# Kernel tuning notes

Hardware: AMD Instinct MI355X
Metric: run time of the kernel (lower is better)

Reference implementation:

```python
import jax, jax.numpy as jnp
import numpy as np

CELL = 14
NC = 80
BPC = 3
IMG = 448.0
CS = IMG / CELL  # cell pixel size
CLASS_SCALE = 1.0
OBJECT_SCALE = 1.0
NOOBJECT_SCALE = 0.5
COORD_SCALE = 5.0
EPS = 1e-9

# base_boxes[y, x, b, :] = (x*CS, y*CS, 0, 0)
_gy, _gx = jnp.meshgrid(jnp.arange(CELL, dtype=jnp.float32), jnp.arange(CELL, dtype=jnp.float32), indexing='ij')
BASE = jnp.broadcast_to(jnp.stack([_gx * CS, _gy * CS, jnp.zeros_like(_gx), jnp.zeros_like(_gx)], axis=-1)[:, :, None, :], (CELL, CELL, BPC, 4))
MULT = jnp.array([CS, CS, IMG, IMG], dtype=jnp.float32)


def _ciou(boxes1, box2):
    # boxes1: [S,S,BPC,4] (cx,cy,w,h); box2: [4]
    b1_cx, b1_cy, b1_w, b1_h = boxes1[..., 0], boxes1[..., 1], boxes1[..., 2], boxes1[..., 3]
    b2_cx, b2_cy, b2_w, b2_h = box2[0], box2[1], box2[2], box2[3]
    b1_x1, b1_y1, b1_x2, b1_y2 = b1_cx - b1_w / 2, b1_cy - b1_h / 2, b1_cx + b1_w / 2, b1_cy + b1_h / 2
    b2_x1, b2_y1, b2_x2, b2_y2 = b2_cx - b2_w / 2, b2_cy - b2_h / 2, b2_cx + b2_w / 2, b2_cy + b2_h / 2
    inter = jnp.clip(jnp.minimum(b1_x2, b2_x2) - jnp.maximum(b1_x1, b2_x1), 0) * \
            jnp.clip(jnp.minimum(b1_y2, b2_y2) - jnp.maximum(b1_y1, b2_y1), 0)
    union = b1_w * b1_h + b2_w * b2_h - inter
    iou = inter / (union + EPS)
    center_distance = (b1_cx - b2_cx) ** 2 + (b1_cy - b2_cy) ** 2
    # faithful to original (uses center/size components for the enclosing box)
    enclose_left = jnp.minimum(boxes1[..., 0], box2[0])
    enclose_right = jnp.maximum(boxes1[..., 2], box2[2])
    enclose_top = jnp.minimum(boxes1[..., 1], box2[1])
    enclose_bottom = jnp.maximum(boxes1[..., 3], box2[3])
    enclose_diag = (enclose_right - enclose_left) ** 2 + (enclose_bottom - enclose_top) ** 2
    v = (4.0 / jnp.pi ** 2) * (jnp.arctan(b2_w / (b2_h + EPS)) - jnp.arctan(b1_w / (b1_h + EPS))) ** 2
    alpha = jax.lax.stop_gradient(v / (1 - iou + v + EPS))
    return iou - center_distance / (enclose_diag + EPS) - alpha * v  # [S,S,BPC]


def _l2(t):
    return 0.5 * jnp.sum(t * t)


def _per_object_loss(predict, label):
    # predict: [S,S,NC+5*BPC], label: [5]
    gy = jnp.arange(CELL, dtype=jnp.float32)[:, None]
    gx = jnp.arange(CELL, dtype=jnp.float32)[None, :]
    x, y, w, h = label[0], label[1], label[2], label[3]
    min_x = jnp.floor((x - w / 2) / CS)
    max_x = jnp.minimum(jnp.ceil((x + w / 2) / CS), CELL)
    min_y = jnp.floor((y - h / 2) / CS)
    max_y = jnp.minimum(jnp.ceil((y + h / 2) / CS), CELL)
    object_mask = ((gx >= min_x) & (gx < max_x) & (gy >= min_y) & (gy < max_y)).astype(jnp.float32)
    cx, cy = jnp.floor(x / CS), jnp.floor(y / CS)
    center_mask = ((gx == cx) & (gy == cy)).astype(jnp.float32)

    pboxes = predict[:, :, NC + BPC:].reshape(CELL, CELL, BPC, 4) * MULT + BASE
    iou = _ciou(pboxes, label[:4])                     # [S,S,BPC]
    C = iou * center_mask[..., None]
    I = (iou >= jnp.max(iou, axis=-1, keepdims=True)).astype(jnp.float32) * center_mask[..., None]
    no_I = 1.0 - I
    p_C = predict[:, :, NC:NC + BPC]

    sqrt_w, sqrt_h = jnp.sqrt(jnp.abs(w)), jnp.sqrt(jnp.abs(h))
    p_x, p_y = pboxes[..., 0], pboxes[..., 1]
    p_sqrt_w = jnp.sqrt(jnp.clip(pboxes[..., 2], 0.0, IMG))
    p_sqrt_h = jnp.sqrt(jnp.clip(pboxes[..., 3], 0.0, IMG))

    P = jax.nn.one_hot(label[4].astype(jnp.int32), NC, dtype=jnp.float32)
    p_P = predict[:, :, :NC]

    class_loss = _l2(object_mask[..., None] * (p_P - P)) * CLASS_SCALE
    object_loss = _l2(I * (p_C - C)) * OBJECT_SCALE
    noobject_loss = _l2(no_I * p_C) * NOOBJECT_SCALE
    coord_loss = (_l2(I * (p_x - x) / CS) + _l2(I * (p_y - y) / CS)
                  + _l2(I * (p_sqrt_w - sqrt_w)) / IMG + _l2(I * (p_sqrt_h - sqrt_h)) / IMG) * COORD_SCALE
    return class_loss + object_loss + noobject_loss + coord_loss


def setup_inputs() -> dict:
    key = jax.random.key(0)
    k1, k2, k3, k4, k5 = jax.random.split(key, 5)
    B, M = 1024, 30
    predicts = jax.random.normal(k1, (B, CELL, CELL, NC + 5 * BPC), dtype=jnp.float32) * 0.1
    xy = jax.random.uniform(k2, (B, M, 2), minval=60.0, maxval=IMG - 60.0)
    wh = jax.random.uniform(k3, (B, M, 2), minval=10.0, maxval=100.0)
    cls = jax.random.randint(k4, (B, M, 1), 0, NC).astype(jnp.float32)
    labels = jnp.concatenate([xy, wh, cls], axis=-1)
    objects_num = jax.random.randint(k5, (B,), 1, M + 1).astype(jnp.int32)
    return {"predicts": predicts, "labels": labels, "objects_num": objects_num}


def reference(predicts, labels, objects_num):
    B, M = labels.shape[0], labels.shape[1]
    per_batch = jax.vmap(lambda p, ls: jax.vmap(lambda l: _per_object_loss(p, l))(ls))
    losses = per_batch(predicts, labels)  # [B, M]
    mask = (jnp.arange(M)[None, :] < objects_num[:, None]).astype(jnp.float32)
    return jnp.sum(losses * mask) / B
```

## Files before the change

kernel.cpp:

```cpp
#include <hip/hip_runtime.h>
#include <math.h>

#define CELLN 14
#define NCELLS 196
#define NCLS 80
#define NCH 95
#define NDW (NCELLS * NCH)
#define NF4 (NDW / 4)

__global__ __launch_bounds__(256, 4) void yolo_loss_kernel(
    const float* __restrict__ predicts,
    const float* __restrict__ labels,
    const int* __restrict__ objects_num,
    float* __restrict__ out,
    int M, float invB)
{
    __shared__ float s_half[NCELLS + 1];
    __shared__ float s_red[4];

    const int img  = blockIdx.x;
    const int tid  = threadIdx.x;
    const int lane = tid & 63;
    const int wid  = tid >> 6;
    const float inv32 = 1.0f / 32.0f;

    const float*  gpred = predicts + (size_t)img * NDW;
    const float4* gp4   = (const float4*)gpred;
    const int n = objects_num[img];

    for (int i = tid; i < NCELLS + 1; i += 256) s_half[i] = 0.0f;
    __syncthreads();

    float acc = 0.0f;
    for (int g = (tid >> 3); g < n; g += 32) {
        const int r = tid & 7;
        const float* lab = labels + ((size_t)img * M + g) * 5;
        const float x = lab[0], y = lab[1], w = lab[2], h = lab[3];

        int min_x = max(0, (int)floorf((x - w * 0.5f) * inv32));
        int max_x = min(CELLN, (int)ceilf((x + w * 0.5f) * inv32));
        int min_y = max(0, (int)floorf((y - h * 0.5f) * inv32));
        int max_y = min(CELLN, (int)ceilf((y + h * 0.5f) * inv32));
        int nx = max_x - min_x;
        int ncell = nx * (max_y - min_y);

        if (r == 0) acc += 0.5f * (float)ncell;
        for (int p = r; p < ncell; p += 8) {
            int cell = (min_y + p / nx) * CELLN + (min_x + p % nx);
            atomicAdd(&s_half[cell], 0.5f);
        }
    }
    __syncthreads();

    const float qn = 0.25f * (float)n;
    float acc2 = 0.0f;
    #pragma unroll
    for (int i = 0; i < 19; ++i) {
        int f = tid + (i << 8);
        if (f < NF4) {
            float4 v4 = gp4[f];
            unsigned idx  = (unsigned)f << 2;
            unsigned cell = idx / 95u;
            unsigned ch   = idx - cell * 95u;
            float vv[4] = {v4.x, v4.y, v4.z, v4.w};
            #pragma unroll
            for (int k = 0; k < 4; ++k) {
                float cnt = s_half[cell];
                float c = (ch < 80u) ? cnt : ((ch < 83u) ? qn : 0.0f);
                float v = vv[k];
                if (k & 1) acc2 = fmaf(c * v, v, acc2);
                else       acc  = fmaf(c * v, v, acc);
                ++ch;
                if (ch == 95u) { ch = 0u; ++cell; }
            }
        }
    }
    acc += acc2;

    for (int g = (tid >> 3); g < n; g += 32) {
        const int r = tid & 7;
        const float* lab = labels + ((size_t)img * M + g) * 5;
        const float x = lab[0], y = lab[1], w = lab[2], h = lab[3];
        const int cls = (int)lab[4];

        int min_x = max(0, (int)floorf((x - w * 0.5f) * inv32));
        int max_x = min(CELLN, (int)ceilf((x + w * 0.5f) * inv32));
        int min_y = max(0, (int)floorf((y - h * 0.5f) * inv32));
        int max_y = min(CELLN, (int)ceilf((y + h * 0.5f) * inv32));
        int nx = max_x - min_x;
        int ncell = nx * (max_y - min_y);

        float csum = 0.0f;
        for (int p = r; p < ncell; p += 8) {
            int cell = (min_y + p / nx) * CELLN + (min_x + p % nx);
            csum += gpred[cell * NCH + cls];
        }
        acc -= csum;
    }

    for (int o = tid; o < n; o += 256) {
        const float* lab = labels + ((size_t)img * M + o) * 5;
        const float x = lab[0], y = lab[1], w = lab[2], h = lab[3];

        int cx = (int)floorf(x * inv32);
        int cy = (int)floorf(y * inv32);
        const float* cp = gpred + (cy * CELLN + cx) * NCH;
        float bx = (float)cx * 32.0f;
        float by = (float)cy * 32.0f;

        float pC[3], ciou[3], pxv[3], pyv[3], pwv[3], phv[3];
        #pragma unroll
        for (int b = 0; b < 3; ++b) {
            pC[b] = cp[NCLS + b];
            float px = cp[83 + 4*b] * 32.0f + bx;
            float py = cp[84 + 4*b] * 32.0f + by;
            float pw = cp[85 + 4*b] * 448.0f;
            float ph = cp[86 + 4*b] * 448.0f;
            pxv[b] = px; pyv[b] = py; pwv[b] = pw; phv[b] = ph;
            float iw = fminf(px + pw*0.5f, x + w*0.5f) - fmaxf(px - pw*0.5f, x - w*0.5f);
            float ih = fminf(py + ph*0.5f, y + h*0.5f) - fmaxf(py - ph*0.5f, y - h*0.5f);
            iw = fmaxf(iw, 0.0f); ih = fmaxf(ih, 0.0f);
            float inter = iw * ih;
            float uni = pw*ph + w*h - inter;
            float iou = inter / (uni + 1e-9f);
            float cd = (px - x)*(px - x) + (py - y)*(py - y);
            float el = fminf(px, x), er = fmaxf(pw, w);
            float et = fminf(py, y), eb = fmaxf(ph, h);
            float ed = (er - el)*(er - el) + (eb - et)*(eb - et);
            float da = atanf(w / (h + 1e-9f)) - atanf(pw / (ph + 1e-9f));
            float v = 0.40528473456935108577f * da * da;
            float alpha = v / (1.0f - iou + v + 1e-9f);
            ciou[b] = iou - cd / (ed + 1e-9f) - alpha * v;
        }
        float mx = fmaxf(ciou[0], fmaxf(ciou[1], ciou[2]));
        float sqw = sqrtf(fabsf(w)), sqh = sqrtf(fabsf(h));
        float sel_obj = 0.0f, sel_pc2 = 0.0f, coord = 0.0f;
        #pragma unroll
        for (int b = 0; b < 3; ++b) {
            if (ciou[b] >= mx) {
                float d = pC[b] - ciou[b];
                sel_obj += d * d;
                sel_pc2 += pC[b] * pC[b];
                float dx = (pxv[b] - x) * inv32;
                float dy = (pyv[b] - y) * inv32;
                float psw = sqrtf(fminf(fmaxf(pwv[b], 0.0f), 448.0f));
                float psh = sqrtf(fminf(fmaxf(phv[b], 0.0f), 448.0f));
                float dw = psw - sqw, dh = psh - sqh;
                coord += dx*dx + dy*dy + (dw*dw + dh*dh) * (1.0f/448.0f);
            }
        }
        acc += 0.5f * sel_obj - 0.25f * sel_pc2 + 2.5f * coord;
    }

    #pragma unroll
    for (int off = 32; off; off >>= 1) acc += __shfl_down(acc, off);
    if (lane == 0) s_red[wid] = acc;
    __syncthreads();
    if (tid == 0) {
        atomicAdd(out, (s_red[0] + s_red[1] + s_red[2] + s_red[3]) * invB);
    }
}

extern "C" void kernel_launch(void* const* d_in, const int* in_sizes, int n_in,
                              void* d_out, int out_size, void* d_ws, size_t ws_size,
                              hipStream_t stream) {
    const float* predicts = (const float*)d_in[0];
    const float* labels   = (const float*)d_in[1];
    const int*   objn     = (const int*)d_in[2];
    float* out = (float*)d_out;

    const int B = in_sizes[2];
    const int M = in_sizes[1] / (B * 5);

    yolo_loss_kernel<<<dim3(B), dim3(256), 0, stream>>>(
        predicts, labels, objn, out, M, 1.0f / (float)B);
}
```

Before: 119.1 us.

## Split each image across two blocks, prefetch predictions, reduce via workspace

Each image is now handled by two blocks, each covering half of the prediction tensor. Each block issues all of its float4 loads into registers up front, before building the shared cell-count table, so the memory traffic overlaps with the atomic setup. Label-driven class and box terms run only in the first half-block, which leaves the two blocks unevenly loaded, and both halves rebuild the shared count table. Per-block partials are written to a workspace and summed by a second single-block kernel instead of a global atomic, which adds one kernel launch.

```diff
diff --git a/kernel.cpp b/kernel.cpp
--- a/kernel.cpp
+++ b/kernel.cpp
@@ -7,18 +7,21 @@
 #define NCH 95
 #define NDW (NCELLS * NCH)
 #define NF4 (NDW / 4)
-
-__global__ __launch_bounds__(256, 4) void yolo_loss_kernel(
+#define HALF0 2328
+
+__global__ __launch_bounds__(256, 4) void yolo_main(
     const float* __restrict__ predicts,
     const float* __restrict__ labels,
     const int* __restrict__ objects_num,
-    float* __restrict__ out,
-    int M, float invB)
+    float* __restrict__ ws,
+    int M)
 {
-    __shared__ float s_half[NCELLS + 1];
+    __shared__ float s_half[NCELLS + 2];
     __shared__ float s_red[4];
 
-    const int img  = blockIdx.x;
+    const int blk  = blockIdx.x;
+    const int img  = blk >> 1;
+    const int sub  = blk & 1;
     const int tid  = threadIdx.x;
     const int lane = tid & 63;
     const int wid  = tid >> 6;
@@ -28,12 +31,23 @@
     const float4* gp4   = (const float4*)gpred;
     const int n = objects_num[img];
 
-    for (int i = tid; i < NCELLS + 1; i += 256) s_half[i] = 0.0f;
+    const int base = sub ? HALF0 : 0;
+    const int C    = sub ? (NF4 - HALF0) : HALF0;
+    const int f0   = base + tid;
+    float4 r[10];
+    #pragma unroll
+    for (int i = 0; i < 9; ++i)
+        r[i] = gp4[f0 + i * 256];
+    const bool ok9 = (tid + 9 * 256) < C;
+    r[9] = gp4[ok9 ? (f0 + 9 * 256) : base];
+    if (!ok9) r[9] = make_float4(0.f, 0.f, 0.f, 0.f);
+
+    for (int i = tid; i < NCELLS + 2; i += 256) s_half[i] = 0.0f;
     __syncthreads();
 
     float acc = 0.0f;
     for (int g = (tid >> 3); g < n; g += 32) {
-        const int r = tid & 7;
+        const int r8 = tid & 7;
         const float* lab = labels + ((size_t)img * M + g) * 5;
         const float x = lab[0], y = lab[1], w = lab[2], h = lab[3];
 
@@ -44,8 +58,8 @@
         int nx = max_x - min_x;
         int ncell = nx * (max_y - min_y);
 
-        if (r == 0) acc += 0.5f * (float)ncell;
-        for (int p = r; p < ncell; p += 8) {
+        if (r8 == 0 && sub == 0) acc += 0.5f * (float)ncell;
+        for (int p = r8; p < ncell; p += 8) {
             int cell = (min_y + p / nx) * CELLN + (min_x + p % nx);
             atomicAdd(&s_half[cell], 0.5f);
         }
@@ -55,110 +69,122 @@
     const float qn = 0.25f * (float)n;
     float acc2 = 0.0f;
     #pragma unroll
-    for (int i = 0; i < 19; ++i) {
-        int f = tid + (i << 8);
-        if (f < NF4) {
-            float4 v4 = gp4[f];
-            unsigned idx  = (unsigned)f << 2;
-            unsigned cell = idx / 95u;
-            unsigned ch   = idx - cell * 95u;
-            float vv[4] = {v4.x, v4.y, v4.z, v4.w};
-            #pragma unroll
-            for (int k = 0; k < 4; ++k) {
-                float cnt = s_half[cell];
-                float c = (ch < 80u) ? cnt : ((ch < 83u) ? qn : 0.0f);
-                float v = vv[k];
-                if (k & 1) acc2 = fmaf(c * v, v, acc2);
-                else       acc  = fmaf(c * v, v, acc);
-                ++ch;
-                if (ch == 95u) { ch = 0u; ++cell; }
-            }
+    for (int i = 0; i < 10; ++i) {
+        unsigned fg = (unsigned)(f0 - base + i * 256);
+        fg += (unsigned)base;
+        if (i == 9) fg = min(fg, (unsigned)(NF4 - 1));
+        unsigned idx  = fg << 2;
+        unsigned cell = idx / 95u;
+        unsigned ch   = idx - cell * 95u;
+        float vv[4] = {r[i].x, r[i].y, r[i].z, r[i].w};
+        #pragma unroll
+        for (int k = 0; k < 4; ++k) {
+            float cnt = s_half[cell];
+            float c = (ch < 80u) ? cnt : ((ch < 83u) ? qn : 0.0f);
+            float v = vv[k];
+            if (k & 1) acc2 = fmaf(c * v, v, acc2);
+            else       acc  = fmaf(c * v, v, acc);
+            ++ch;
+            if (ch == 95u) { ch = 0u; ++cell; }
         }
     }
     acc += acc2;
 
-    for (int g = (tid >> 3); g < n; g += 32) {
-        const int r = tid & 7;
-        const float* lab = labels + ((size_t)img * M + g) * 5;
-        const float x = lab[0], y = lab[1], w = lab[2], h = lab[3];
-        const int cls = (int)lab[4];
-
-        int min_x = max(0, (int)floorf((x - w * 0.5f) * inv32));
-        int max_x = min(CELLN, (int)ceilf((x + w * 0.5f) * inv32));
-        int min_y = max(0, (int)floorf((y - h * 0.5f) * inv32));
-        int max_y = min(CELLN, (int)ceilf((y + h * 0.5f) * inv32));
-        int nx = max_x - min_x;
-        int ncell = nx * (max_y - min_y);
-
-        float csum = 0.0f;
-        for (int p = r; p < ncell; p += 8) {
-            int cell = (min_y + p / nx) * CELLN + (min_x + p % nx);
-            csum += gpred[cell * NCH + cls];
-        }
-        acc -= csum;
-    }
-
-    for (int o = tid; o < n; o += 256) {
-        const float* lab = labels + ((size_t)img * M + o) * 5;
-        const float x = lab[0], y = lab[1], w = lab[2], h = lab[3];
-
-        int cx = (int)floorf(x * inv32);
-        int cy = (int)floorf(y * inv32);
-        const float* cp = gpred + (cy * CELLN + cx) * NCH;
-        float bx = (float)cx * 32.0f;
-        float by = (float)cy * 32.0f;
-
-        float pC[3], ciou[3], pxv[3], pyv[3], pwv[3], phv[3];
-        #pragma unroll
-        for (int b = 0; b < 3; ++b) {
-            pC[b] = cp[NCLS + b];
-            float px = cp[83 + 4*b] * 32.0f + bx;
-            float py = cp[84 + 4*b] * 32.0f + by;
-            float pw = cp[85 + 4*b] * 448.0f;
-            float ph = cp[86 + 4*b] * 448.0f;
-            pxv[b] = px; pyv[b] = py; pwv[b] = pw; phv[b] = ph;
-            float iw = fminf(px + pw*0.5f, x + w*0.5f) - fmaxf(px - pw*0.5f, x - w*0.5f);
-            float ih = fminf(py + ph*0.5f, y + h*0.5f) - fmaxf(py - ph*0.5f, y - h*0.5f);
-            iw = fmaxf(iw, 0.0f); ih = fmaxf(ih, 0.0f);
-            float inter = iw * ih;
-            float uni = pw*ph + w*h - inter;
-            float iou = inter / (uni + 1e-9f);
-            float cd = (px - x)*(px - x) + (py - y)*(py - y);
-            float el = fminf(px, x), er = fmaxf(pw, w);
-            float et = fminf(py, y), eb = fmaxf(ph, h);
-            float ed = (er - el)*(er - el) + (eb - et)*(eb - et);
-            float da = atanf(w / (h + 1e-9f)) - atanf(pw / (ph + 1e-9f));
-            float v = 0.40528473456935108577f * da * da;
-            float alpha = v / (1.0f - iou + v + 1e-9f);
-            ciou[b] = iou - cd / (ed + 1e-9f) - alpha * v;
-        }
-        float mx = fmaxf(ciou[0], fmaxf(ciou[1], ciou[2]));
-        float sqw = sqrtf(fabsf(w)), sqh = sqrtf(fabsf(h));
-        float sel_obj = 0.0f, sel_pc2 = 0.0f, coord = 0.0f;
-        #pragma unroll
-        for (int b = 0; b < 3; ++b) {
-            if (ciou[b] >= mx) {
-                float d = pC[b] - ciou[b];
-                sel_obj += d * d;
-                sel_pc2 += pC[b] * pC[b];
-                float dx = (pxv[b] - x) * inv32;
-                float dy = (pyv[b] - y) * inv32;
-                float psw = sqrtf(fminf(fmaxf(pwv[b], 0.0f), 448.0f));
-                float psh = sqrtf(fminf(fmaxf(phv[b], 0.0f), 448.0f));
-                float dw = psw - sqw, dh = psh - sqh;
-                coord += dx*dx + dy*dy + (dw*dw + dh*dh) * (1.0f/448.0f);
+    if (sub == 0) {
+        for (int g = (tid >> 3); g < n; g += 32) {
+            const int r8 = tid & 7;
+            const float* lab = labels + ((size_t)img * M + g) * 5;
+            const float x = lab[0], y = lab[1], w = lab[2], h = lab[3];
+            const int cls = (int)lab[4];
+
+            int min_x = max(0, (int)floorf((x - w * 0.5f) * inv32));
+            int max_x = min(CELLN, (int)ceilf((x + w * 0.5f) * inv32));
+            int min_y = max(0, (int)floorf((y - h * 0.5f) * inv32));
+            int max_y = min(CELLN, (int)ceilf((y + h * 0.5f) * inv32));
+            int nx = max_x - min_x;
+            int ncell = nx * (max_y - min_y);
+
+            float csum = 0.0f;
+            for (int p = r8; p < ncell; p += 8) {
+                int cell = (min_y + p / nx) * CELLN + (min_x + p % nx);
+                csum += gpred[cell * NCH + cls];
             }
-        }
-        acc += 0.5f * sel_obj - 0.25f * sel_pc2 + 2.5f * coord;
+            acc -= csum;
+        }
+
+        for (int o = tid; o < n; o += 256) {
+            const float* lab = labels + ((size_t)img * M + o) * 5;
+            const float x = lab[0], y = lab[1], w = lab[2], h = lab[3];
+
+            int cx = (int)floorf(x * inv32);
+            int cy = (int)floorf(y * inv32);
+            const float* cp = gpred + (cy * CELLN + cx) * NCH;
+            float bx = (float)cx * 32.0f;
+            float by = (float)cy * 32.0f;
+
+            float pC[3], ciou[3], pxv[3], pyv[3], pwv[3], phv[3];
+            #pragma unroll
+            for (int b = 0; b < 3; ++b) {
+                pC[b] = cp[NCLS + b];
+                float px = cp[83 + 4*b] * 32.0f + bx;
+                float py = cp[84 + 4*b] * 32.0f + by;
+                float pw = cp[85 + 4*b] * 448.0f;
+                float ph = cp[86 + 4*b] * 448.0f;
+                pxv[b] = px; pyv[b] = py; pwv[b] = pw; phv[b] = ph;
+                float iw = fminf(px + pw*0.5f, x + w*0.5f) - fmaxf(px - pw*0.5f, x - w*0.5f);
+                float ih = fminf(py + ph*0.5f, y + h*0.5f) - fmaxf(py - ph*0.5f, y - h*0.5f);
+                iw = fmaxf(iw, 0.0f); ih = fmaxf(ih, 0.0f);
+                float inter = iw * ih;
+                float uni = pw*ph + w*h - inter;
+                float iou = inter / (uni + 1e-9f);
+                float cd = (px - x)*(px - x) + (py - y)*(py - y);
+                float el = fminf(px, x), er = fmaxf(pw, w);
+                float et = fminf(py, y), eb = fmaxf(ph, h);
+                float ed = (er - el)*(er - el) + (eb - et)*(eb - et);
+                float da = atanf(w / (h + 1e-9f)) - atanf(pw / (ph + 1e-9f));
+                float v = 0.40528473456935108577f * da * da;
+                float alpha = v / (1.0f - iou + v + 1e-9f);
+                ciou[b] = iou - cd / (ed + 1e-9f) - alpha * v;
+            }
+            float mx = fmaxf(ciou[0], fmaxf(ciou[1], ciou[2]));
+            float sqw = sqrtf(fabsf(w)), sqh = sqrtf(fabsf(h));
+            float sel_obj = 0.0f, sel_pc2 = 0.0f, coord = 0.0f;
+            #pragma unroll
+            for (int b = 0; b < 3; ++b) {
+                if (ciou[b] >= mx) {
+                    float d = pC[b] - ciou[b];
+                    sel_obj += d * d;
+                    sel_pc2 += pC[b] * pC[b];
+                    float dx = (pxv[b] - x) * inv32;
+                    float dy = (pyv[b] - y) * inv32;
+                    float psw = sqrtf(fminf(fmaxf(pwv[b], 0.0f), 448.0f));
+                    float psh = sqrtf(fminf(fmaxf(phv[b], 0.0f), 448.0f));
+                    float dw = psw - sqw, dh = psh - sqh;
+                    coord += dx*dx + dy*dy + (dw*dw + dh*dh) * (1.0f/448.0f);
+                }
+            }
+            acc += 0.5f * sel_obj - 0.25f * sel_pc2 + 2.5f * coord;
+        }
     }
 
     #pragma unroll
     for (int off = 32; off; off >>= 1) acc += __shfl_down(acc, off);
     if (lane == 0) s_red[wid] = acc;
     __syncthreads();
-    if (tid == 0) {
-        atomicAdd(out, (s_red[0] + s_red[1] + s_red[2] + s_red[3]) * invB);
-    }
+    if (tid == 0) ws[blk] = s_red[0] + s_red[1] + s_red[2] + s_red[3];
+}
+
+__global__ __launch_bounds__(256) void yolo_reduce(
+    const float* __restrict__ ws, float* __restrict__ out, int nP, float invB)
+{
+    __shared__ float s_red[4];
+    float a = 0.0f;
+    for (int i = threadIdx.x; i < nP; i += 256) a += ws[i];
+    #pragma unroll
+    for (int off = 32; off; off >>= 1) a += __shfl_down(a, off);
+    if ((threadIdx.x & 63) == 0) s_red[threadIdx.x >> 6] = a;
+    __syncthreads();
+    if (threadIdx.x == 0) out[0] = (s_red[0] + s_red[1] + s_red[2] + s_red[3]) * invB;
 }
 
 extern "C" void kernel_launch(void* const* d_in, const int* in_sizes, int n_in,
@@ -168,10 +194,12 @@
     const float* labels   = (const float*)d_in[1];
     const int*   objn     = (const int*)d_in[2];
     float* out = (float*)d_out;
+    float* ws  = (float*)d_ws;
 
     const int B = in_sizes[2];
     const int M = in_sizes[1] / (B * 5);
-
-    yolo_loss_kernel<<<dim3(B), dim3(256), 0, stream>>>(
-        predicts, labels, objn, out, M, 1.0f / (float)B);
+    const int nBlk = 2 * B;
+
+    yolo_main<<<dim3(nBlk), dim3(256), 0, stream>>>(predicts, labels, objn, ws, M);
+    yolo_reduce<<<dim3(1), dim3(256), 0, stream>>>(ws, out, nBlk, 1.0f / (float)B);
 }
```

New measurement: 115.0 us. 1.04x faster.
